# Kernel optimization log

Hardware: AMD Instinct MI355X
Metric: run time of the kernel (lower is better)

## Reference

```python
import jax, jax.numpy as jnp
import numpy as np

N_NODES = 100000
N_HYPEREDGES = 50000
FEAT_DIM = 64
N_MEMBERS = 1000000  # total (hyperedge, node) membership pairs, ragged groups


def setup_inputs() -> dict:
    key = jax.random.key(0)
    k1, k2, k3 = jax.random.split(key, 3)
    # node feature table (features_mat, i.e. an nn.Embedding weight)
    features = jax.random.normal(k1, (N_NODES, FEAT_DIM), dtype=jnp.float32)
    # flattened hyp2nodes: node id of each membership pair
    node_ids = jax.random.randint(k2, (N_MEMBERS,), 0, N_NODES, dtype=jnp.int64)
    # hyperedge id of each membership pair (sorted, like concatenated per-edge lists)
    segment_ids = jnp.sort(
        jax.random.randint(k3, (N_MEMBERS,), 0, N_HYPEREDGES, dtype=jnp.int64)
    )
    return {
        "features": features,
        "node_ids": node_ids,
        "segment_ids": segment_ids,
        "num_segments": N_HYPEREDGES,
    }


def reference(features, node_ids, segment_ids, num_segments):
    # compute(): for each hyperedge, gather its member node features and max-reduce.
    gathered = features[node_ids]  # [E, F] ragged gather
    # fused ragged segment-max (what the torch loop / mask-broadcast emulates)
    embed_matrix = jax.ops.segment_max(
        gathered, segment_ids, num_segments=num_segments
    )  # [M, F]
    return embed_matrix
```

## Files before the change

### kernel.cpp

```cpp
#include <hip/hip_runtime.h>
#include <math.h>

#define FEAT 64
#define SEGS_PER_BLOCK 4

static __device__ __forceinline__ ushort f32_to_bf16_rne(float f) {
    uint32_t u = __float_as_uint(f);
    uint32_t r = (u + 0x7fffu + ((u >> 16) & 1u)) >> 16;
    return (ushort)r;
}

__device__ __forceinline__ float4 fmax4(float4 a, float4 b) {
    return make_float4(fmaxf(a.x, b.x), fmaxf(a.y, b.y),
                       fmaxf(a.z, b.z), fmaxf(a.w, b.w));
}

__global__ __launch_bounds__(256)
void pre_kernel(const float* __restrict__ feat,
                const int* __restrict__ segment_ids,
                ushort* __restrict__ feat_bf,
                int* __restrict__ starts,
                int conv_blocks, int n_elems, int n_members, int num_segments) {
    if ((int)blockIdx.x < conv_blocks) {
        const int e0 = (blockIdx.x * 256 + threadIdx.x) << 3;
        if (e0 < n_elems) {
            const float4 a = *(const float4*)(feat + e0);
            const float4 b = *(const float4*)(feat + e0 + 4);
            uint4 o;
            o.x = (uint)f32_to_bf16_rne(a.x) | ((uint)f32_to_bf16_rne(a.y) << 16);
            o.y = (uint)f32_to_bf16_rne(a.z) | ((uint)f32_to_bf16_rne(a.w) << 16);
            o.z = (uint)f32_to_bf16_rne(b.x) | ((uint)f32_to_bf16_rne(b.y) << 16);
            o.w = (uint)f32_to_bf16_rne(b.z) | ((uint)f32_to_bf16_rne(b.w) << 16);
            *(uint4*)(feat_bf + e0) = o;
        }
    } else {
        const int t  = (blockIdx.x - conv_blocks) * 256 + threadIdx.x;
        const int j0 = t << 2;
        if (j0 >= n_members) return;
        const int4 s4 = *(const int4*)(segment_ids + j0);
        int prev = (j0 == 0) ? -1 : segment_ids[j0 - 1];
        const int vals[4] = {s4.x, s4.y, s4.z, s4.w};
        #pragma unroll
        for (int k = 0; k < 4; ++k) {
            const int j = j0 + k;
            if (j < n_members) {
                const int sj = vals[k];
                for (int s = prev + 1; s <= sj; ++s) starts[s] = j;
                prev = sj;
            }
        }
        if (j0 + 4 >= n_members) {
            for (int s = prev + 1; s <= num_segments; ++s) starts[s] = n_members;
        }
    }
}

__global__ __launch_bounds__(64 * SEGS_PER_BLOCK)
void HyperedgeMaxAggregator_kernel(const ushort* __restrict__ feat_bf,
                                   const int* __restrict__ node_ids,
                                   const int* __restrict__ starts,
                                   float* __restrict__ out,
                                   int num_segments) {
    const int wave = threadIdx.x >> 6;
    const int lane = threadIdx.x & 63;
    const int seg  = blockIdx.x * SEGS_PER_BLOCK + wave;
    if (seg >= num_segments) return;

    const int start = starts[seg];
    const int end   = starts[seg + 1];

    const int mslot = lane >> 3;
    const int fo    = (lane & 7) << 3;

    float acc[8];
    #pragma unroll
    for (int k = 0; k < 8; ++k) acc[k] = -INFINITY;

    int base = start;
    int cnt  = end - start;
    while (cnt > 0) {
        const int take = (cnt < 64) ? cnt : 64;
        const int myid = (lane < take) ? node_ids[base + lane] : 0;
        #pragma unroll
        for (int s = 0; s < 8; ++s) {
            const int j  = (s << 3) + mslot;
            const int id = __shfl(myid, j, 64);
            const uint4 v = *(const uint4*)(feat_bf + (size_t)id * FEAT + fo);
            if (j < take) {
                const uint w[4] = {v.x, v.y, v.z, v.w};
                #pragma unroll
                for (int q = 0; q < 4; ++q) {
                    acc[2*q]   = fmaxf(acc[2*q],   __uint_as_float(w[q] << 16));
                    acc[2*q+1] = fmaxf(acc[2*q+1], __uint_as_float(w[q] & 0xffff0000u));
                }
            }
        }
        base += take;
        cnt  -= take;
    }

    #pragma unroll
    for (int d = 8; d <= 32; d <<= 1) {
        #pragma unroll
        for (int k = 0; k < 8; ++k) {
            acc[k] = fmaxf(acc[k], __shfl_xor(acc[k], d, 64));
        }
    }

    if (lane < 8) {
        float* op = out + (size_t)seg * FEAT + (lane << 3);
        *(float4*)(op)     = make_float4(acc[0], acc[1], acc[2], acc[3]);
        *(float4*)(op + 4) = make_float4(acc[4], acc[5], acc[6], acc[7]);
    }
}

__global__ __launch_bounds__(256)
void seg_starts_kernel(const int* __restrict__ segment_ids,
                       int* __restrict__ starts,
                       int n_members, int num_segments) {
    const int j = blockIdx.x * blockDim.x + threadIdx.x;
    if (j >= n_members) return;
    const int sj = segment_ids[j];
    const int sp = (j == 0) ? -1 : segment_ids[j - 1];
    for (int s = sp + 1; s <= sj; ++s) starts[s] = j;
    if (j == n_members - 1) {
        for (int s = sj + 1; s <= num_segments; ++s) starts[s] = n_members;
    }
}

__global__ __launch_bounds__(64 * SEGS_PER_BLOCK)
void hyper_max_f32(const float* __restrict__ features,
                   const int* __restrict__ node_ids,
                   const int* __restrict__ starts,
                   float* __restrict__ out,
                   int num_segments) {
    const int wave = threadIdx.x >> 6;
    const int lane = threadIdx.x & 63;
    const int seg  = blockIdx.x * SEGS_PER_BLOCK + wave;
    if (seg >= num_segments) return;
    const int start = starts[seg];
    const int end   = starts[seg + 1];
    const int mslot = lane >> 4;
    const int fq    = (lane & 15) << 2;
    float4 acc = make_float4(-INFINITY, -INFINITY, -INFINITY, -INFINITY);
    for (int j = start + mslot; j < end; j += 4) {
        const int n0 = node_ids[j];
        acc = fmax4(acc, *(const float4*)(features + (size_t)n0 * FEAT + fq));
    }
    acc.x = fmaxf(acc.x, __shfl_xor(acc.x, 16, 64));
    acc.y = fmaxf(acc.y, __shfl_xor(acc.y, 16, 64));
    acc.z = fmaxf(acc.z, __shfl_xor(acc.z, 16, 64));
    acc.w = fmaxf(acc.w, __shfl_xor(acc.w, 16, 64));
    acc.x = fmaxf(acc.x, __shfl_xor(acc.x, 32, 64));
    acc.y = fmaxf(acc.y, __shfl_xor(acc.y, 32, 64));
    acc.z = fmaxf(acc.z, __shfl_xor(acc.z, 32, 64));
    acc.w = fmaxf(acc.w, __shfl_xor(acc.w, 32, 64));
    if (lane < 16) *(float4*)(out + (size_t)seg * FEAT + fq) = acc;
}

extern "C" void kernel_launch(void* const* d_in, const int* in_sizes, int n_in,
                              void* d_out, int out_size, void* d_ws, size_t ws_size,
                              hipStream_t stream) {
    const float* features    = (const float*)d_in[0];
    const int*   node_ids    = (const int*)d_in[1];
    const int*   segment_ids = (const int*)d_in[2];
    float* out = (float*)d_out;

    const int n_elems      = in_sizes[0];
    const int n_members    = in_sizes[1];
    const int num_segments = out_size / FEAT;

    const size_t starts_bytes = (((size_t)(num_segments + 1) * 4) + 255) & ~(size_t)255;
    const size_t bf_bytes     = (size_t)n_elems * 2;
    int* starts = (int*)d_ws;

    const int seg_blocks = (num_segments + SEGS_PER_BLOCK - 1) / SEGS_PER_BLOCK;

    if (ws_size >= starts_bytes + bf_bytes) {
        ushort* feat_bf = (ushort*)((char*)d_ws + starts_bytes);
        const int conv_blocks   = ((n_elems >> 3) + 255) / 256;
        const int starts_blocks = (((n_members + 3) >> 2) + 255) / 256;
        pre_kernel<<<conv_blocks + starts_blocks, 256, 0, stream>>>(
            features, segment_ids, feat_bf, starts,
            conv_blocks, n_elems, n_members, num_segments);
        HyperedgeMaxAggregator_kernel<<<seg_blocks, 64 * SEGS_PER_BLOCK, 0, stream>>>(
            feat_bf, node_ids, starts, out, num_segments);
    } else {
        seg_starts_kernel<<<(n_members + 255) / 256, 256, 0, stream>>>(
            segment_ids, starts, n_members, num_segments);
        hyper_max_f32<<<seg_blocks, 64 * SEGS_PER_BLOCK, 0, stream>>>(
            features, node_ids, starts, out, num_segments);
    }
}
```

Baseline: 40.33 us.

## Use persistent grid-stride waves with prefetch of next segment's indices

The main aggregation kernel now runs a capped grid of 2048 blocks in which each wave loops over segments with a grid stride. While it reduces the current segment, it prefetches the next segment's start/end offsets and first 64 node ids, hiding that dependent-load latency. The feature conversion in the pre-kernel now uses nontemporal loads, and launch bounds ask for a minimum occupancy of 8 blocks. The cost is added register pressure and possibly fewer waves in flight than with one wave per segment, which could reduce latency hiding for the gathers.

```diff
diff --git a/kernel.cpp b/kernel.cpp
--- a/kernel.cpp
+++ b/kernel.cpp
@@ -3,16 +3,14 @@
 
 #define FEAT 64
 #define SEGS_PER_BLOCK 4
+#define MAIN_BLOCKS 2048
+
+typedef float floatx4 __attribute__((ext_vector_type(4)));
 
 static __device__ __forceinline__ ushort f32_to_bf16_rne(float f) {
     uint32_t u = __float_as_uint(f);
     uint32_t r = (u + 0x7fffu + ((u >> 16) & 1u)) >> 16;
     return (ushort)r;
-}
-
-__device__ __forceinline__ float4 fmax4(float4 a, float4 b) {
-    return make_float4(fmaxf(a.x, b.x), fmaxf(a.y, b.y),
-                       fmaxf(a.z, b.z), fmaxf(a.w, b.w));
 }
 
 __global__ __launch_bounds__(256)
@@ -24,8 +22,9 @@
     if ((int)blockIdx.x < conv_blocks) {
         const int e0 = (blockIdx.x * 256 + threadIdx.x) << 3;
         if (e0 < n_elems) {
-            const float4 a = *(const float4*)(feat + e0);
-            const float4 b = *(const float4*)(feat + e0 + 4);
+            const floatx4* p = (const floatx4*)(feat + e0);
+            const floatx4 a = __builtin_nontemporal_load(p);
+            const floatx4 b = __builtin_nontemporal_load(p + 1);
             uint4 o;
             o.x = (uint)f32_to_bf16_rne(a.x) | ((uint)f32_to_bf16_rne(a.y) << 16);
             o.y = (uint)f32_to_bf16_rne(a.z) | ((uint)f32_to_bf16_rne(a.w) << 16);
@@ -55,32 +54,39 @@
     }
 }
 
-__global__ __launch_bounds__(64 * SEGS_PER_BLOCK)
+__global__ __launch_bounds__(64 * SEGS_PER_BLOCK, 8)
 void HyperedgeMaxAggregator_kernel(const ushort* __restrict__ feat_bf,
                                    const int* __restrict__ node_ids,
                                    const int* __restrict__ starts,
                                    float* __restrict__ out,
-                                   int num_segments) {
+                                   int num_segments, int stride) {
     const int wave = threadIdx.x >> 6;
     const int lane = threadIdx.x & 63;
-    const int seg  = blockIdx.x * SEGS_PER_BLOCK + wave;
+    int seg = blockIdx.x * SEGS_PER_BLOCK + wave;
     if (seg >= num_segments) return;
-
-    const int start = starts[seg];
-    const int end   = starts[seg + 1];
 
     const int mslot = lane >> 3;
     const int fo    = (lane & 7) << 3;
 
-    float acc[8];
-    #pragma unroll
-    for (int k = 0; k < 8; ++k) acc[k] = -INFINITY;
-
-    int base = start;
-    int cnt  = end - start;
-    while (cnt > 0) {
-        const int take = (cnt < 64) ? cnt : 64;
-        const int myid = (lane < take) ? node_ids[base + lane] : 0;
+    int st = starts[seg];
+    int en = starts[seg + 1];
+    int myid = (lane < en - st) ? node_ids[st + lane] : 0;
+
+    while (true) {
+        const int seg2 = seg + stride;
+        int st2 = 0, en2 = 0, myid2 = 0;
+        if (seg2 < num_segments) {
+            st2 = starts[seg2];
+            en2 = starts[seg2 + 1];
+            myid2 = (lane < en2 - st2) ? node_ids[st2 + lane] : 0;
+        }
+
+        float acc[8];
+        #pragma unroll
+        for (int k = 0; k < 8; ++k) acc[k] = -INFINITY;
+
+        int take = en - st;
+        if (take > 64) take = 64;
         #pragma unroll
         for (int s = 0; s < 8; ++s) {
             const int j  = (s << 3) + mslot;
@@ -95,22 +101,45 @@
                 }
             }
         }
-        base += take;
-        cnt  -= take;
-    }
-
-    #pragma unroll
-    for (int d = 8; d <= 32; d <<= 1) {
-        #pragma unroll
-        for (int k = 0; k < 8; ++k) {
-            acc[k] = fmaxf(acc[k], __shfl_xor(acc[k], d, 64));
-        }
-    }
-
-    if (lane < 8) {
-        float* op = out + (size_t)seg * FEAT + (lane << 3);
-        *(float4*)(op)     = make_float4(acc[0], acc[1], acc[2], acc[3]);
-        *(float4*)(op + 4) = make_float4(acc[4], acc[5], acc[6], acc[7]);
+
+        int base = st + 64;
+        while (base < en) {
+            int t2 = en - base;
+            if (t2 > 64) t2 = 64;
+            const int mid = (lane < t2) ? node_ids[base + lane] : 0;
+            #pragma unroll
+            for (int s = 0; s < 8; ++s) {
+                const int j  = (s << 3) + mslot;
+                const int id = __shfl(mid, j, 64);
+                const uint4 v = *(const uint4*)(feat_bf + (size_t)id * FEAT + fo);
+                if (j < t2) {
+                    const uint w[4] = {v.x, v.y, v.z, v.w};
+                    #pragma unroll
+                    for (int q = 0; q < 4; ++q) {
+                        acc[2*q]   = fmaxf(acc[2*q],   __uint_as_float(w[q] << 16));
+                        acc[2*q+1] = fmaxf(acc[2*q+1], __uint_as_float(w[q] & 0xffff0000u));
+                    }
+                }
+            }
+            base += 64;
+        }
+
+        #pragma unroll
+        for (int d = 8; d <= 32; d <<= 1) {
+            #pragma unroll
+            for (int k = 0; k < 8; ++k) {
+                acc[k] = fmaxf(acc[k], __shfl_xor(acc[k], d, 64));
+            }
+        }
+
+        if (lane < 8) {
+            float* op = out + (size_t)seg * FEAT + (lane << 3);
+            *(float4*)(op)     = make_float4(acc[0], acc[1], acc[2], acc[3]);
+            *(float4*)(op + 4) = make_float4(acc[4], acc[5], acc[6], acc[7]);
+        }
+
+        if (seg2 >= num_segments) break;
+        seg = seg2; st = st2; en = en2; myid = myid2;
     }
 }
 
@@ -145,7 +174,9 @@
     float4 acc = make_float4(-INFINITY, -INFINITY, -INFINITY, -INFINITY);
     for (int j = start + mslot; j < end; j += 4) {
         const int n0 = node_ids[j];
-        acc = fmax4(acc, *(const float4*)(features + (size_t)n0 * FEAT + fq));
+        const float4 v = *(const float4*)(features + (size_t)n0 * FEAT + fq);
+        acc.x = fmaxf(acc.x, v.x); acc.y = fmaxf(acc.y, v.y);
+        acc.z = fmaxf(acc.z, v.z); acc.w = fmaxf(acc.w, v.w);
     }
     acc.x = fmaxf(acc.x, __shfl_xor(acc.x, 16, 64));
     acc.y = fmaxf(acc.y, __shfl_xor(acc.y, 16, 64));
@@ -183,8 +214,11 @@
         pre_kernel<<<conv_blocks + starts_blocks, 256, 0, stream>>>(
             features, segment_ids, feat_bf, starts,
             conv_blocks, n_elems, n_members, num_segments);
-        HyperedgeMaxAggregator_kernel<<<seg_blocks, 64 * SEGS_PER_BLOCK, 0, stream>>>(
-            feat_bf, node_ids, starts, out, num_segments);
+
+        const int blocks = (seg_blocks < MAIN_BLOCKS) ? seg_blocks : MAIN_BLOCKS;
+        const int stride = blocks * SEGS_PER_BLOCK;
+        HyperedgeMaxAggregator_kernel<<<blocks, 64 * SEGS_PER_BLOCK, 0, stream>>>(
+            feat_bf, node_ids, starts, out, num_segments, stride);
     } else {
         seg_starts_kernel<<<(n_members + 255) / 256, 256, 0, stream>>>(
             segment_ids, starts, n_members, num_segments);
```

Result: slower. 44.48 us (+10.3%).
